# Kernel optimization log

Hardware: AMD Instinct MI355X
Metric: run time of the kernel (lower is better)

Reference implementation:

```python
import jax, jax.numpy as jnp
import numpy as np

N_NODES = 10000
N_EDGES = 640000
IN_CH = 128
HID_CH = 128


def setup_inputs() -> dict:
    key = jax.random.key(0)
    ks = jax.random.split(key, 6)
    x = jax.random.normal(ks[0], (N_NODES, IN_CH), dtype=jnp.float32)
    edge_index = jax.random.randint(ks[1], (2, N_EDGES), 0, N_NODES, dtype=jnp.int32)
    # GCNConv weights (glorot-ish scale) and biases
    W1 = jax.random.normal(ks[2], (IN_CH, HID_CH), dtype=jnp.float32) / np.float32(np.sqrt(IN_CH))
    b1 = jnp.zeros((HID_CH,), jnp.float32)
    W2 = jax.random.normal(ks[3], (HID_CH, HID_CH), dtype=jnp.float32) / np.float32(np.sqrt(HID_CH))
    b2 = jnp.zeros((HID_CH,), jnp.float32)
    prelu_a = jnp.full((HID_CH,), 0.25, jnp.float32)  # nn.PReLU(hidden) init
    return {"x": x, "edge_index": edge_index, "W1": W1, "b1": b1,
            "W2": W2, "b2": b2, "prelu_a": prelu_a}


def _gcn_conv(x, W, b, src, dst, norm, n_nodes):
    # x: [N, Fin] -> transform, gather by src, scale by sym-norm, scatter-add to dst
    h = x @ W                                   # [N, Fout]
    msg = h[src] * norm[:, None]                # [E+N, Fout] gather (irregular)
    out = jax.ops.segment_sum(msg, dst, num_segments=n_nodes)
    return out + b


def reference(x, edge_index, W1, b1, W2, b2, prelu_a):
    n = x.shape[0]
    # PyG GCNConv default: add self-loops, symmetric D^{-1/2} A D^{-1/2} norm
    loops = jnp.arange(n, dtype=edge_index.dtype)
    src = jnp.concatenate([edge_index[0], loops])
    dst = jnp.concatenate([edge_index[1], loops])
    deg = jax.ops.segment_sum(jnp.ones_like(dst, dtype=jnp.float32), dst,
                              num_segments=n)
    dinv = jax.lax.rsqrt(jnp.maximum(deg, 1.0))  # deg >= 1 due to self-loops
    norm = dinv[src] * dinv[dst]                 # [E+N]

    h = _gcn_conv(x, W1, b1, src, dst, norm, n)
    h = jnp.where(h > 0, h, prelu_a * h)         # per-channel PReLU
    # Dropout(p=0.1) is identity in eval mode (correctness baseline)
    out = _gcn_conv(h, W2, b2, src, dst, norm, n)
    return out
```

## Files before the change

kernel.cpp:

```cpp
#include <hip/hip_runtime.h>

#define CH 128
#define HALF_CAP 96
#define ROW_ENT 192
#define CSTRIDE 32
#define GFILL 2048

typedef float    fvec4 __attribute__((ext_vector_type(4)));
typedef float    fvec2 __attribute__((ext_vector_type(2)));
typedef unsigned uvec4 __attribute__((ext_vector_type(4)));
typedef unsigned uvec2 __attribute__((ext_vector_type(2)));

__device__ __forceinline__ unsigned short f2bf(float f) {
    union { float f; unsigned int u; } v; v.f = f;
    unsigned int u = v.u;
    u += 0x7FFFu + ((u >> 16) & 1u);
    return (unsigned short)(u >> 16);
}
__device__ __forceinline__ float bflo(unsigned int p) {
    union { unsigned int u; float f; } v; v.u = p << 16; return v.f;
}
__device__ __forceinline__ float bfhi(unsigned int p) {
    union { unsigned int u; float f; } v; v.u = p & 0xFFFF0000u; return v.f;
}

__global__ __launch_bounds__(256, 5) void fg2_kernel(const int* __restrict__ src,
                                                     const int* __restrict__ dst,
                                                     int* __restrict__ cursor,
                                                     unsigned short* __restrict__ slots,
                                                     int E,
                                                     const float* __restrict__ A,
                                                     const float* __restrict__ W,
                                                     float* __restrict__ C,
                                                     int M, int ngb) {
    __shared__ float Ws[128 * 64];
    int bid = blockIdx.x, t = threadIdx.x;
    if (bid >= ngb) {
        int e0 = (bid - ngb) * 256 + t;
        int stride = GFILL * 256;
        for (int e = e0; e < E; e += stride) {
            int d = __builtin_nontemporal_load(dst + e);
            int s = __builtin_nontemporal_load(src + e);
            int p = e & 1;
            int r = atomicAdd(&cursor[((size_t)d * 2 + p) * CSTRIDE], 1);
            if (r < HALF_CAP)
                slots[(size_t)d * ROW_ENT + p * HALF_CAP + r] = (unsigned short)s;
        }
        return;
    }
    int tile = bid >> 1;
    int c0 = (bid & 1) * 64;
    fvec4* Ws4 = (fvec4*)Ws;
    const fvec4* Wg = (const fvec4*)W;
#pragma unroll
    for (int i = 0; i < 8; ++i) {
        int idx = t + i * 256;
        int k = idx >> 4, c = idx & 15;
        Ws4[idx] = Wg[k * 32 + (c0 >> 2) + c];
    }
    __syncthreads();
    int rg = t >> 4, cg = t & 15;
    int row0 = tile * 32 + rg * 2;
    bool v0 = row0 < M, v1 = row0 + 1 < M;
    const fvec4* Ar0 = (const fvec4*)(A + (size_t)(v0 ? row0 : 0) * CH);
    const fvec4* Ar1 = (const fvec4*)(A + (size_t)(v1 ? row0 + 1 : 0) * CH);
    fvec4 acc0 = {0.f,0.f,0.f,0.f}, acc1 = {0.f,0.f,0.f,0.f};
#pragma unroll 4
    for (int k4 = 0; k4 < 32; ++k4) {
        fvec4 a0 = Ar0[k4], a1 = Ar1[k4];
#pragma unroll
        for (int j = 0; j < 4; ++j) {
            fvec4 w = Ws4[(k4 * 4 + j) * 16 + cg];
            acc0 += a0[j] * w;
            acc1 += a1[j] * w;
        }
    }
    if (v0) ((fvec4*)(C + (size_t)row0 * CH + c0))[cg] = acc0;
    if (v1) ((fvec4*)(C + (size_t)(row0 + 1) * CH + c0))[cg] = acc1;
}

__global__ __launch_bounds__(256) void scale_kernel(const float* __restrict__ C,
                                                    const int* __restrict__ cursor,
                                                    unsigned short* __restrict__ Cb,
                                                    int N) {
    int row = blockIdx.x * 4 + (threadIdx.x >> 6);
    if (row >= N) return;
    int lane = threadIdx.x & 63;
    int c0 = cursor[(size_t)row * 2 * CSTRIDE];
    int c1 = cursor[((size_t)row * 2 + 1) * CSTRIDE];
    float dn = rsqrtf((float)(c0 + c1 + 1));
    fvec2 v = ((const fvec2*)(C + (size_t)row * CH))[lane];
    unsigned pk = ((unsigned)f2bf(dn * v.y) << 16) | (unsigned)f2bf(dn * v.x);
    ((unsigned*)(Cb + (size_t)row * CH))[lane] = pk;
}

__global__ __launch_bounds__(256, 5) void gemm2_kernel(const float* __restrict__ A,
                                                       const float* __restrict__ W,
                                                       const int* __restrict__ deg,
                                                       float* __restrict__ C,
                                                       unsigned short* __restrict__ Cb,
                                                       int M) {
    __shared__ float Ws[128 * 64];
    int t = threadIdx.x;
    int tile = blockIdx.x >> 1;
    int c0 = (blockIdx.x & 1) * 64;
    fvec4* Ws4 = (fvec4*)Ws;
    const fvec4* Wg = (const fvec4*)W;
#pragma unroll
    for (int i = 0; i < 8; ++i) {
        int idx = t + i * 256;
        int k = idx >> 4, c = idx & 15;
        Ws4[idx] = Wg[k * 32 + (c0 >> 2) + c];
    }
    __syncthreads();
    int rg = t >> 4, cg = t & 15;
    int row0 = tile * 32 + rg * 2;
    bool v0 = row0 < M, v1 = row0 + 1 < M;
    const fvec4* Ar0 = (const fvec4*)(A + (size_t)(v0 ? row0 : 0) * CH);
    const fvec4* Ar1 = (const fvec4*)(A + (size_t)(v1 ? row0 + 1 : 0) * CH);
    fvec4 acc0 = {0.f,0.f,0.f,0.f}, acc1 = {0.f,0.f,0.f,0.f};
#pragma unroll 4
    for (int k4 = 0; k4 < 32; ++k4) {
        fvec4 a0 = Ar0[k4], a1 = Ar1[k4];
#pragma unroll
        for (int j = 0; j < 4; ++j) {
            fvec4 w = Ws4[(k4 * 4 + j) * 16 + cg];
            acc0 += a0[j] * w;
            acc1 += a1[j] * w;
        }
    }
#pragma unroll
    for (int r = 0; r < 2; ++r) {
        bool v = r ? v1 : v0;
        if (!v) continue;
        int rr = row0 + r;
        fvec4 s = r ? acc1 : acc0;
        int d0 = deg[(size_t)rr * 2 * CSTRIDE];
        int d1 = deg[((size_t)rr * 2 + 1) * CSTRIDE];
        float dn = rsqrtf((float)(d0 + d1 + 1));
        ((fvec4*)(C + (size_t)rr * CH + c0))[cg] = s;
        ((ushort4*)(Cb + (size_t)rr * CH + c0))[cg] =
            make_ushort4(f2bf(dn * s.x), f2bf(dn * s.y),
                         f2bf(dn * s.z), f2bf(dn * s.w));
    }
}

__global__ __launch_bounds__(256) void agg_kernel(const unsigned short* __restrict__ hb,
                                                  const float* __restrict__ hf,
                                                  const unsigned short* __restrict__ slots,
                                                  const int* __restrict__ cursor,
                                                  const float* __restrict__ bias,
                                                  const float* __restrict__ prelu_a,
                                                  float* __restrict__ outp,
                                                  int N, int apply_prelu) {
    int wave = threadIdx.x >> 6, lane = threadIdx.x & 63;
    int node = blockIdx.x * 4 + wave;
    if (node >= N) return;
    int half = lane >> 5, sl = lane & 31;
    int dgh = cursor[((size_t)node * 2 + half) * CSTRIDE];
    int dtot = dgh + __shfl_xor(dgh, 32);
    if (dgh > HALF_CAP) dgh = HALF_CAP;
    const unsigned short* sp = slots + (size_t)node * ROW_ENT + half * HALF_CAP;
    const unsigned short* hbl = hb + 4 * sl;
    float a0 = 0.f, a1 = 0.f, a2 = 0.f, a3 = 0.f;
    int k = 0;
    for (; k + 16 <= dgh; k += 16) {
        uvec4 qa = *(const uvec4*)(sp + k);
        uvec4 qb = *(const uvec4*)(sp + k + 8);
        unsigned q[8] = {qa.x, qa.y, qa.z, qa.w, qb.x, qb.y, qb.z, qb.w};
        uvec2 p[16];
#pragma unroll
        for (int j = 0; j < 8; ++j) {
            unsigned lo = q[j] & 0xFFFFu, hi = q[j] >> 16;
            p[2 * j]     = *(const uvec2*)(hbl + (size_t)lo * CH);
            p[2 * j + 1] = *(const uvec2*)(hbl + (size_t)hi * CH);
        }
#pragma unroll
        for (int j = 0; j < 16; ++j) {
            a0 += bflo(p[j].x); a1 += bfhi(p[j].x);
            a2 += bflo(p[j].y); a3 += bfhi(p[j].y);
        }
    }
    if (k < dgh) {
        uvec4 qa = *(const uvec4*)(sp + k);
        uvec4 qb = *(const uvec4*)(sp + k + 8);
        unsigned q[8] = {qa.x, qa.y, qa.z, qa.w, qb.x, qb.y, qb.z, qb.w};
#pragma unroll
        for (int j = 0; j < 8; ++j) {
            unsigned lo = q[j] & 0xFFFFu, hi = q[j] >> 16;
            lo = lo < (unsigned)N ? lo : 0u;
            hi = hi < (unsigned)N ? hi : 0u;
            uvec2 plo = *(const uvec2*)(hbl + (size_t)lo * CH);
            uvec2 phi = *(const uvec2*)(hbl + (size_t)hi * CH);
            if (k + 2 * j < dgh) {
                a0 += bflo(plo.x); a1 += bfhi(plo.x);
                a2 += bflo(plo.y); a3 += bfhi(plo.y);
            }
            if (k + 2 * j + 1 < dgh) {
                a0 += bflo(phi.x); a1 += bfhi(phi.x);
                a2 += bflo(phi.y); a3 += bfhi(phi.y);
            }
        }
    }
    a0 += __shfl_xor(a0, 32);
    a1 += __shfl_xor(a1, 32);
    a2 += __shfl_xor(a2, 32);
    a3 += __shfl_xor(a3, 32);
    if (half == 0) {
        float dn = rsqrtf((float)(dtot + 1));
        float d2 = dn * dn;
        fvec4 hv = ((const fvec4*)(hf + (size_t)node * CH))[sl];
        fvec4 bv = ((const fvec4*)bias)[sl];
        float r0 = dn * a0 + d2 * hv.x + bv.x;
        float r1 = dn * a1 + d2 * hv.y + bv.y;
        float r2 = dn * a2 + d2 * hv.z + bv.z;
        float r3 = dn * a3 + d2 * hv.w + bv.w;
        if (apply_prelu) {
            fvec4 av = ((const fvec4*)prelu_a)[sl];
            r0 = r0 > 0.f ? r0 : av.x * r0;
            r1 = r1 > 0.f ? r1 : av.y * r1;
            r2 = r2 > 0.f ? r2 : av.z * r2;
            r3 = r3 > 0.f ? r3 : av.w * r3;
        }
        fvec4 rv = {r0, r1, r2, r3};
        ((fvec4*)(outp + (size_t)node * CH))[sl] = rv;
    }
}


extern "C" void kernel_launch(void* const* d_in, const int* in_sizes, int n_in,
                              void* d_out, int out_size, void* d_ws, size_t ws_size,
                              hipStream_t stream) {
    const float* x  = (const float*)d_in[0];
    const int*   ei = (const int*)d_in[1];
    const float* W1 = (const float*)d_in[2];
    const float* b1 = (const float*)d_in[3];
    const float* W2 = (const float*)d_in[4];
    const float* b2 = (const float*)d_in[5];
    const float* pa = (const float*)d_in[6];

    int N = in_sizes[0] / CH;
    int E = in_sizes[1] / 2;
    const int* src = ei;
    const int* dst = ei + E;

    char* w = (char*)d_ws;
    auto alloc = [&](size_t bytes) {
        void* p = (void*)w;
        w += (bytes + 255) & ~(size_t)255;
        return p;
    };
    int*            cursor = (int*)alloc((size_t)N * 2 * CSTRIDE * 4);
    unsigned short* slots  = (unsigned short*)alloc((size_t)N * ROW_ENT * 2);
    float*          bufA   = (float*)alloc((size_t)N * CH * 4);
    unsigned short* bufAb  = (unsigned short*)alloc((size_t)N * CH * 2);
    float*          bufB   = (float*)alloc((size_t)N * CH * 4);
    float*          outp   = (float*)d_out;

    int ntiles = (N + 31) / 32;
    int ngb = 2 * ntiles;

    hipMemsetAsync(cursor, 0, (size_t)N * 2 * CSTRIDE * 4, stream);

    fg2_kernel<<<ngb + GFILL, 256, 0, stream>>>(src, dst, cursor, slots, E, x, W1, bufA, N, ngb);
    scale_kernel<<<(N + 3) / 4, 256, 0, stream>>>(bufA, cursor, bufAb, N);
    agg_kernel<<<(N + 3) / 4, 256, 0, stream>>>(bufAb, bufA, slots, cursor, b1, pa, bufB, N, 1);

    gemm2_kernel<<<ngb, 256, 0, stream>>>(bufB, W2, cursor, bufA, bufAb, N);
    agg_kernel<<<(N + 3) / 4, 256, 0, stream>>>(bufAb, bufA, slots, cursor, b2, pa, outp, N, 0);
}
```

Baseline: 169.1 us.

## Replace global-atomic CSR fill with two-pass bucket partition and local build

Builds the adjacency slots in two passes. The first pass partitions edges into 64-node buckets, using shared-memory counters and one global atomic per bucket per block. The second pass builds per-node slot lists with shared atomics and writes a compact degree array. This removes per-edge global atomics on padded cursors. In exchange the GEMM no longer overlaps with the fill, because the first GEMM now runs after the build and fuses the scaling step, so scale_kernel is dropped. It also adds an extra bucket buffer round trip, and the aggregation now has each half-wave gather alternate slots.

```diff
diff --git a/kernel.cpp b/kernel.cpp
--- a/kernel.cpp
+++ b/kernel.cpp
@@ -1,13 +1,15 @@
 #include <hip/hip_runtime.h>
 
 #define CH 128
-#define HALF_CAP 96
-#define ROW_ENT 192
+#define SLOT_CAP 128
+#define BSHIFT 6
+#define BNODES 64
+#define MAXB 256
+#define CAPB 4608
 #define CSTRIDE 32
-#define GFILL 2048
+#define EPB 2048
 
 typedef float    fvec4 __attribute__((ext_vector_type(4)));
-typedef float    fvec2 __attribute__((ext_vector_type(2)));
 typedef unsigned uvec4 __attribute__((ext_vector_type(4)));
 typedef unsigned uvec2 __attribute__((ext_vector_type(2)));
 
@@ -24,77 +26,73 @@
     union { unsigned int u; float f; } v; v.u = p & 0xFFFF0000u; return v.f;
 }
 
-__global__ __launch_bounds__(256, 5) void fg2_kernel(const int* __restrict__ src,
-                                                     const int* __restrict__ dst,
-                                                     int* __restrict__ cursor,
-                                                     unsigned short* __restrict__ slots,
-                                                     int E,
-                                                     const float* __restrict__ A,
-                                                     const float* __restrict__ W,
-                                                     float* __restrict__ C,
-                                                     int M, int ngb) {
-    __shared__ float Ws[128 * 64];
-    int bid = blockIdx.x, t = threadIdx.x;
-    if (bid >= ngb) {
-        int e0 = (bid - ngb) * 256 + t;
-        int stride = GFILL * 256;
-        for (int e = e0; e < E; e += stride) {
+__global__ __launch_bounds__(256) void part_kernel(const int* __restrict__ src,
+                                                   const int* __restrict__ dst,
+                                                   int* __restrict__ bcur,
+                                                   unsigned* __restrict__ bbuf,
+                                                   int E, int nb) {
+    __shared__ int cnt[MAXB];
+    __shared__ int base[MAXB];
+    int t = threadIdx.x;
+    for (int i = t; i < nb; i += 256) cnt[i] = 0;
+    __syncthreads();
+    int e0 = blockIdx.x * EPB;
+    unsigned pkt[8];
+    int rk[8];
+#pragma unroll
+    for (int i = 0; i < 8; ++i) {
+        int e = e0 + i * 256 + t;
+        pkt[i] = 0xFFFFFFFFu;
+        rk[i] = -1;
+        if (e < E) {
             int d = __builtin_nontemporal_load(dst + e);
             int s = __builtin_nontemporal_load(src + e);
-            int p = e & 1;
-            int r = atomicAdd(&cursor[((size_t)d * 2 + p) * CSTRIDE], 1);
-            if (r < HALF_CAP)
-                slots[(size_t)d * ROW_ENT + p * HALF_CAP + r] = (unsigned short)s;
-        }
-        return;
-    }
-    int tile = bid >> 1;
-    int c0 = (bid & 1) * 64;
-    fvec4* Ws4 = (fvec4*)Ws;
-    const fvec4* Wg = (const fvec4*)W;
+            pkt[i] = (unsigned)d | ((unsigned)s << 16);
+            rk[i] = atomicAdd(&cnt[d >> BSHIFT], 1);
+        }
+    }
+    __syncthreads();
+    for (int b = t; b < nb; b += 256) {
+        int c = cnt[b];
+        base[b] = c ? atomicAdd(&bcur[(size_t)b * CSTRIDE], c) : 0;
+    }
+    __syncthreads();
 #pragma unroll
     for (int i = 0; i < 8; ++i) {
-        int idx = t + i * 256;
-        int k = idx >> 4, c = idx & 15;
-        Ws4[idx] = Wg[k * 32 + (c0 >> 2) + c];
-    }
-    __syncthreads();
-    int rg = t >> 4, cg = t & 15;
-    int row0 = tile * 32 + rg * 2;
-    bool v0 = row0 < M, v1 = row0 + 1 < M;
-    const fvec4* Ar0 = (const fvec4*)(A + (size_t)(v0 ? row0 : 0) * CH);
-    const fvec4* Ar1 = (const fvec4*)(A + (size_t)(v1 ? row0 + 1 : 0) * CH);
-    fvec4 acc0 = {0.f,0.f,0.f,0.f}, acc1 = {0.f,0.f,0.f,0.f};
-#pragma unroll 4
-    for (int k4 = 0; k4 < 32; ++k4) {
-        fvec4 a0 = Ar0[k4], a1 = Ar1[k4];
-#pragma unroll
-        for (int j = 0; j < 4; ++j) {
-            fvec4 w = Ws4[(k4 * 4 + j) * 16 + cg];
-            acc0 += a0[j] * w;
-            acc1 += a1[j] * w;
-        }
-    }
-    if (v0) ((fvec4*)(C + (size_t)row0 * CH + c0))[cg] = acc0;
-    if (v1) ((fvec4*)(C + (size_t)(row0 + 1) * CH + c0))[cg] = acc1;
-}
-
-__global__ __launch_bounds__(256) void scale_kernel(const float* __restrict__ C,
-                                                    const int* __restrict__ cursor,
-                                                    unsigned short* __restrict__ Cb,
+        if (rk[i] < 0) continue;
+        int b = (pkt[i] & 0xFFFFu) >> BSHIFT;
+        int idx = base[b] + rk[i];
+        if (idx < CAPB) bbuf[(size_t)b * CAPB + idx] = pkt[i];
+    }
+}
+
+__global__ __launch_bounds__(256) void build_kernel(const unsigned* __restrict__ bbuf,
+                                                    const int* __restrict__ bcur,
+                                                    unsigned short* __restrict__ slots,
+                                                    int* __restrict__ deg,
                                                     int N) {
-    int row = blockIdx.x * 4 + (threadIdx.x >> 6);
-    if (row >= N) return;
-    int lane = threadIdx.x & 63;
-    int c0 = cursor[(size_t)row * 2 * CSTRIDE];
-    int c1 = cursor[((size_t)row * 2 + 1) * CSTRIDE];
-    float dn = rsqrtf((float)(c0 + c1 + 1));
-    fvec2 v = ((const fvec2*)(C + (size_t)row * CH))[lane];
-    unsigned pk = ((unsigned)f2bf(dn * v.y) << 16) | (unsigned)f2bf(dn * v.x);
-    ((unsigned*)(Cb + (size_t)row * CH))[lane] = pk;
-}
-
-__global__ __launch_bounds__(256, 5) void gemm2_kernel(const float* __restrict__ A,
+    __shared__ int lcnt[BNODES];
+    int b = blockIdx.x, t = threadIdx.x;
+    if (t < BNODES) lcnt[t] = 0;
+    __syncthreads();
+    int cnt = bcur[(size_t)b * CSTRIDE];
+    if (cnt > CAPB) cnt = CAPB;
+    const unsigned* bp = bbuf + (size_t)b * CAPB;
+    for (int i = t; i < cnt; i += 256) {
+        unsigned pkt = bp[i];
+        int d = pkt & 0xFFFFu;
+        int r = atomicAdd(&lcnt[d - (b << BSHIFT)], 1);
+        if (r < SLOT_CAP)
+            slots[((size_t)d << 7) + r] = (unsigned short)(pkt >> 16);
+    }
+    __syncthreads();
+    if (t < BNODES) {
+        int node = (b << BSHIFT) + t;
+        if (node < N) deg[node] = lcnt[t];
+    }
+}
+
+__global__ __launch_bounds__(256, 5) void gemmp_kernel(const float* __restrict__ A,
                                                        const float* __restrict__ W,
                                                        const int* __restrict__ deg,
                                                        float* __restrict__ C,
@@ -135,9 +133,7 @@
         if (!v) continue;
         int rr = row0 + r;
         fvec4 s = r ? acc1 : acc0;
-        int d0 = deg[(size_t)rr * 2 * CSTRIDE];
-        int d1 = deg[((size_t)rr * 2 + 1) * CSTRIDE];
-        float dn = rsqrtf((float)(d0 + d1 + 1));
+        float dn = rsqrtf((float)(deg[rr] + 1));
         ((fvec4*)(C + (size_t)rr * CH + c0))[cg] = s;
         ((ushort4*)(Cb + (size_t)rr * CH + c0))[cg] =
             make_ushort4(f2bf(dn * s.x), f2bf(dn * s.y),
@@ -148,7 +144,7 @@
 __global__ __launch_bounds__(256) void agg_kernel(const unsigned short* __restrict__ hb,
                                                   const float* __restrict__ hf,
                                                   const unsigned short* __restrict__ slots,
-                                                  const int* __restrict__ cursor,
+                                                  const int* __restrict__ deg,
                                                   const float* __restrict__ bias,
                                                   const float* __restrict__ prelu_a,
                                                   float* __restrict__ outp,
@@ -156,49 +152,41 @@
     int wave = threadIdx.x >> 6, lane = threadIdx.x & 63;
     int node = blockIdx.x * 4 + wave;
     if (node >= N) return;
+    int dg = deg[node];
+    if (dg > SLOT_CAP) dg = SLOT_CAP;
     int half = lane >> 5, sl = lane & 31;
-    int dgh = cursor[((size_t)node * 2 + half) * CSTRIDE];
-    int dtot = dgh + __shfl_xor(dgh, 32);
-    if (dgh > HALF_CAP) dgh = HALF_CAP;
-    const unsigned short* sp = slots + (size_t)node * ROW_ENT + half * HALF_CAP;
+    const unsigned short* sp = slots + ((size_t)node << 7);
     const unsigned short* hbl = hb + 4 * sl;
     float a0 = 0.f, a1 = 0.f, a2 = 0.f, a3 = 0.f;
     int k = 0;
-    for (; k + 16 <= dgh; k += 16) {
+    for (; k + 16 <= dg; k += 16) {
         uvec4 qa = *(const uvec4*)(sp + k);
         uvec4 qb = *(const uvec4*)(sp + k + 8);
         unsigned q[8] = {qa.x, qa.y, qa.z, qa.w, qb.x, qb.y, qb.z, qb.w};
-        uvec2 p[16];
+        uvec2 p[8];
 #pragma unroll
         for (int j = 0; j < 8; ++j) {
-            unsigned lo = q[j] & 0xFFFFu, hi = q[j] >> 16;
-            p[2 * j]     = *(const uvec2*)(hbl + (size_t)lo * CH);
-            p[2 * j + 1] = *(const uvec2*)(hbl + (size_t)hi * CH);
-        }
-#pragma unroll
-        for (int j = 0; j < 16; ++j) {
+            unsigned idx = half ? (q[j] >> 16) : (q[j] & 0xFFFFu);
+            p[j] = *(const uvec2*)(hbl + (size_t)idx * CH);
+        }
+#pragma unroll
+        for (int j = 0; j < 8; ++j) {
             a0 += bflo(p[j].x); a1 += bfhi(p[j].x);
             a2 += bflo(p[j].y); a3 += bfhi(p[j].y);
         }
     }
-    if (k < dgh) {
+    if (k < dg) {
         uvec4 qa = *(const uvec4*)(sp + k);
         uvec4 qb = *(const uvec4*)(sp + k + 8);
         unsigned q[8] = {qa.x, qa.y, qa.z, qa.w, qb.x, qb.y, qb.z, qb.w};
 #pragma unroll
         for (int j = 0; j < 8; ++j) {
-            unsigned lo = q[j] & 0xFFFFu, hi = q[j] >> 16;
-            lo = lo < (unsigned)N ? lo : 0u;
-            hi = hi < (unsigned)N ? hi : 0u;
-            uvec2 plo = *(const uvec2*)(hbl + (size_t)lo * CH);
-            uvec2 phi = *(const uvec2*)(hbl + (size_t)hi * CH);
-            if (k + 2 * j < dgh) {
-                a0 += bflo(plo.x); a1 += bfhi(plo.x);
-                a2 += bflo(plo.y); a3 += bfhi(plo.y);
-            }
-            if (k + 2 * j + 1 < dgh) {
-                a0 += bflo(phi.x); a1 += bfhi(phi.x);
-                a2 += bflo(phi.y); a3 += bfhi(phi.y);
+            unsigned raw = half ? (q[j] >> 16) : (q[j] & 0xFFFFu);
+            unsigned idx = raw < (unsigned)N ? raw : 0u;
+            uvec2 pv = *(const uvec2*)(hbl + (size_t)idx * CH);
+            if (k + 2 * j + half < dg) {
+                a0 += bflo(pv.x); a1 += bfhi(pv.x);
+                a2 += bflo(pv.y); a3 += bfhi(pv.y);
             }
         }
     }
@@ -207,7 +195,7 @@
     a2 += __shfl_xor(a2, 32);
     a3 += __shfl_xor(a3, 32);
     if (half == 0) {
-        float dn = rsqrtf((float)(dtot + 1));
+        float dn = rsqrtf((float)(dg + 1));
         float d2 = dn * dn;
         fvec4 hv = ((const fvec4*)(hf + (size_t)node * CH))[sl];
         fvec4 bv = ((const fvec4*)bias)[sl];
@@ -243,6 +231,7 @@
     int E = in_sizes[1] / 2;
     const int* src = ei;
     const int* dst = ei + E;
+    int nb = (N + BNODES - 1) >> BSHIFT;
 
     char* w = (char*)d_ws;
     auto alloc = [&](size_t bytes) {
@@ -250,22 +239,26 @@
         w += (bytes + 255) & ~(size_t)255;
         return p;
     };
-    int*            cursor = (int*)alloc((size_t)N * 2 * CSTRIDE * 4);
-    unsigned short* slots  = (unsigned short*)alloc((size_t)N * ROW_ENT * 2);
+    int*            bcur   = (int*)alloc((size_t)nb * CSTRIDE * 4);
+    unsigned*       bbuf   = (unsigned*)alloc((size_t)nb * CAPB * 4);
+    unsigned short* slots  = (unsigned short*)alloc((size_t)N * SLOT_CAP * 2);
+    int*            deg    = (int*)alloc((size_t)N * 4);
     float*          bufA   = (float*)alloc((size_t)N * CH * 4);
     unsigned short* bufAb  = (unsigned short*)alloc((size_t)N * CH * 2);
     float*          bufB   = (float*)alloc((size_t)N * CH * 4);
     float*          outp   = (float*)d_out;
 
     int ntiles = (N + 31) / 32;
-    int ngb = 2 * ntiles;
-
-    hipMemsetAsync(cursor, 0, (size_t)N * 2 * CSTRIDE * 4, stream);
-
-    fg2_kernel<<<ngb + GFILL, 256, 0, stream>>>(src, dst, cursor, slots, E, x, W1, bufA, N, ngb);
-    scale_kernel<<<(N + 3) / 4, 256, 0, stream>>>(bufA, cursor, bufAb, N);
-    agg_kernel<<<(N + 3) / 4, 256, 0, stream>>>(bufAb, bufA, slots, cursor, b1, pa, bufB, N, 1);
-
-    gemm2_kernel<<<ngb, 256, 0, stream>>>(bufB, W2, cursor, bufA, bufAb, N);
-    agg_kernel<<<(N + 3) / 4, 256, 0, stream>>>(bufAb, bufA, slots, cursor, b2, pa, outp, N, 0);
-}
+    int npb = (E + EPB - 1) / EPB;
+
+    hipMemsetAsync(bcur, 0, (size_t)nb * CSTRIDE * 4, stream);
+
+    part_kernel<<<npb, 256, 0, stream>>>(src, dst, bcur, bbuf, E, nb);
+    build_kernel<<<nb, 256, 0, stream>>>(bbuf, bcur, slots, deg, N);
+
+    gemmp_kernel<<<2 * ntiles, 256, 0, stream>>>(x, W1, deg, bufA, bufAb, N);
+    agg_kernel<<<(N + 3) / 4, 256, 0, stream>>>(bufAb, bufA, slots, deg, b1, pa, bufB, N, 1);
+
+    gemmp_kernel<<<2 * ntiles, 256, 0, stream>>>(bufB, W2, deg, bufA, bufAb, N);
+    agg_kernel<<<(N + 3) / 4, 256, 0, stream>>>(bufAb, bufA, slots, deg, b2, pa, outp, N, 0);
+}
```

After: 150.3 us. 1.12x faster.
